# Performance work log

Hardware: AMD Instinct MI355X
Metric: run time of the kernel (lower is better)

## Reference

```python
import jax, jax.numpy as jnp
import numpy as np

N, D, NUM_CLASSES = 8192, 512, 100

def _col_normalize(z):
    # torch.std default is unbiased (ddof=1)
    mean = z.mean(axis=0)
    std = z.std(axis=0, ddof=1)
    return (z - mean) / std

def setup_inputs() -> dict:
    key = jax.random.key(0)
    k1, k2, k3 = jax.random.split(key, 3)
    z_a = jax.random.normal(k1, (N, D), dtype=jnp.float32)
    z_b = jax.random.normal(k2, (N, D), dtype=jnp.float32)
    labels = jax.random.randint(k3, (N,), 0, NUM_CLASSES, dtype=jnp.int64)
    return {"z_a": z_a, "z_b": z_b, "labels": labels}

def reference(z_a, z_b, labels):
    d = z_a.shape[1]
    z_a_norm = _col_normalize(z_a)
    z_b_norm = _col_normalize(z_b)
    # c: [N, N] cross-correlation between samples
    c = jnp.matmul(z_a_norm, z_b_norm.T) / d
    # m[i, j] = 1 if labels[i] == labels[j] else 0 (replaces per-row loop)
    m = (labels[:, None] == labels[None, :]).astype(c.dtype)
    loss = jnp.sum((c - m) ** 2)
    return loss
```

## Files before the change

kernel.cpp:

```cpp
#include <hip/hip_runtime.h>
#include <math.h>


#define NN 8192
#define DD 512
#define NC 100
#define SPLITK 16
#define NXT 10
#define NTILE 14

#define CPS_B   0u
#define CPQ_B   524288u
#define MUA_B   1048576u
#define MUB_B   1050624u
#define RSA_B   1052672u
#define RSB_B   1054720u
#define CNT_B   1056768u
#define XTA_B   4194304u
#define XTB_B   12582912u
#define MT_B    20971520u
#define PART_B  23068672u

typedef __attribute__((ext_vector_type(8))) short short8;
typedef __attribute__((ext_vector_type(4))) float f32x4;

__constant__ int c_ti[NTILE] = {0,0,0,0,1,1,1,2,2,3, 0,1,2,3};
__constant__ int c_tj[NTILE] = {0,1,2,3,1,2,3,2,3,3, 4,4,4,4};
__constant__ float c_w[NXT]  = {1.f,2.f,2.f,2.f,1.f,2.f,2.f,1.f,2.f,1.f};

#if defined(__has_builtin)
#if __has_builtin(__builtin_amdgcn_global_load_lds)
#define HAVE_GLL 1
#endif
#endif

#ifdef HAVE_GLL
__device__ __forceinline__ void async16(const void* g, void* l) {
    __builtin_amdgcn_global_load_lds(
        (const __attribute__((address_space(1))) void*)g,
        (__attribute__((address_space(3))) void*)l, 16, 0, 0);
}
#endif

__device__ __forceinline__ short f2bf_rne(float f) {
    unsigned int u = __builtin_bit_cast(unsigned int, f);
    u += 0x7fffu + ((u >> 16) & 1u);
    return (short)(u >> 16);
}

__device__ __forceinline__ float block_reduce_sum_p(float v, float* red) {
    int lane = threadIdx.x & 63;
    int wave = threadIdx.x >> 6;
    #pragma unroll
    for (int off = 32; off > 0; off >>= 1) v += __shfl_down(v, off, 64);
    if (lane == 0) red[wave] = v;
    __syncthreads();
    float s = 0.f;
    if (threadIdx.x == 0) {
        int nw = (blockDim.x + 63) >> 6;
        for (int w = 0; w < nw; w++) s += red[w];
    }
    return s;
}

__global__ __launch_bounds__(256) void k_prep(const float* __restrict__ A,
                                              const float* __restrict__ B,
                                              const int* __restrict__ labels,
                                              short* __restrict__ XTa,
                                              short* __restrict__ XTb,
                                              short* __restrict__ MT,
                                              float* __restrict__ cpsum,
                                              float* __restrict__ cpsq,
                                              int* __restrict__ counts,
                                              float* __restrict__ out) {
    __shared__ short LT[64][72];
    __shared__ float WS[4][16][4];
    __shared__ float WQ[4][16][4];
    __shared__ int hist[NC];
    int bid = blockIdx.x;
    int t = threadIdx.x;

    if (bid >= 2048) {
        if (bid >= 2176) {
            if (t < NC) hist[t] = 0;
            __syncthreads();
            for (int i = t; i < NN; i += 256) atomicAdd(&hist[labels[i]], 1);
            __syncthreads();
            if (t < 128) counts[t] = (t < NC) ? hist[t] : 0;
            if (t == 0) out[0] = 0.f;
            return;
        }
        int c = bid - 2048;
        unsigned short one = 0x3F80;
        ushort4* dst = (ushort4*)(MT + (size_t)c * NN);
        const int4* lb4 = (const int4*)labels;
        #pragma unroll
        for (int j = 0; j < 8; j++) {
            int i4 = j * 256 + t;
            int4 lb = lb4[i4];
            ushort4 v;
            v.x = (lb.x == c) ? one : (unsigned short)0;
            v.y = (lb.y == c) ? one : (unsigned short)0;
            v.z = (lb.z == c) ? one : (unsigned short)0;
            v.w = (lb.w == c) ? one : (unsigned short)0;
            dst[i4] = v;
        }
        return;
    }

    int mat = bid >> 10;
    const float* X = mat ? B : A;
    short* XT = mat ? XTb : XTa;
    int rem = bid & 1023;
    int c0 = (rem >> 7) << 6;
    int kb_blk = rem & 127;
    int k0 = kb_blk << 6;
    int cc = t & 15;
    int kb = t >> 4;

    float4 ps = make_float4(0.f, 0.f, 0.f, 0.f);
    float4 pq = make_float4(0.f, 0.f, 0.f, 0.f);
    #pragma unroll
    for (int s = 0; s < 4; s++) {
        int kr = kb + s * 16;
        float4 v = *(const float4*)&X[(size_t)(k0 + kr) * DD + c0 + cc * 4];
        LT[cc * 4 + 0][kr] = f2bf_rne(v.x);
        LT[cc * 4 + 1][kr] = f2bf_rne(v.y);
        LT[cc * 4 + 2][kr] = f2bf_rne(v.z);
        LT[cc * 4 + 3][kr] = f2bf_rne(v.w);
        ps.x += v.x; ps.y += v.y; ps.z += v.z; ps.w += v.w;
        pq.x += v.x * v.x; pq.y += v.y * v.y;
        pq.z += v.z * v.z; pq.w += v.w * v.w;
    }
    #pragma unroll
    for (int off = 16; off <= 32; off <<= 1) {
        ps.x += __shfl_xor(ps.x, off, 64); pq.x += __shfl_xor(pq.x, off, 64);
        ps.y += __shfl_xor(ps.y, off, 64); pq.y += __shfl_xor(pq.y, off, 64);
        ps.z += __shfl_xor(ps.z, off, 64); pq.z += __shfl_xor(pq.z, off, 64);
        ps.w += __shfl_xor(ps.w, off, 64); pq.w += __shfl_xor(pq.w, off, 64);
    }
    int wv = t >> 6, lane = t & 63;
    if (lane < 16) {
        WS[wv][lane][0] = ps.x; WS[wv][lane][1] = ps.y;
        WS[wv][lane][2] = ps.z; WS[wv][lane][3] = ps.w;
        WQ[wv][lane][0] = pq.x; WQ[wv][lane][1] = pq.y;
        WQ[wv][lane][2] = pq.z; WQ[wv][lane][3] = pq.w;
    }
    __syncthreads();

    #pragma unroll
    for (int s = 0; s < 2; s++) {
        int idx = s * 256 + t;
        int orow = idx >> 3;
        int och = idx & 7;
        *(uint4*)&XT[(size_t)(c0 + orow) * NN + k0 + och * 8] =
            *(const uint4*)&LT[orow][och * 8];
    }
    if (t < 64) {
        int ccf = t >> 2, j = t & 3;
        float s = WS[0][ccf][j] + WS[1][ccf][j] + WS[2][ccf][j] + WS[3][ccf][j];
        float q = WQ[0][ccf][j] + WQ[1][ccf][j] + WQ[2][ccf][j] + WQ[3][ccf][j];
        size_t base = ((size_t)mat * 128 + kb_blk) * 512 + c0 + t;
        cpsum[base] = s;
        cpsq[base] = q;
    }
}

__global__ __launch_bounds__(256, 2) void k_gram(const short* __restrict__ XTa,
                                                 const short* __restrict__ XTb,
                                                 const short* __restrict__ MT,
                                                 float* __restrict__ part,
                                                 const float* __restrict__ cpsum,
                                                 const float* __restrict__ cpsq,
                                                 float* __restrict__ mu_a,
                                                 float* __restrict__ mu_b,
                                                 float* __restrict__ rs_a,
                                                 float* __restrict__ rs_b) {
    __shared__ short LA[2][128 * 64];
    __shared__ short LB[2][128 * 64];

    int b = blockIdx.x;
    int t = threadIdx.x;

    if (b >= 448) {
        int mat = b - 448;
        for (int k = t; k < DD; k += 256) {
            float s = 0.f, q = 0.f;
            for (int kb = 0; kb < 128; kb++) {
                size_t base = ((size_t)mat * 128 + kb) * 512 + k;
                s += cpsum[base];
                q += cpsq[base];
            }
            float mu = s * (1.0f / (float)NN);
            float var = (q - (float)NN * mu * mu) / (float)(NN - 1);
            (mat ? mu_b : mu_a)[k] = mu;
            (mat ? rs_b : rs_a)[k] = rsqrtf(var);
        }
        return;
    }

    int xcd = b & 7;
    int idx = b >> 3;
    int grp = (idx / NTILE) * 8 + xcd;
    int tile = idx % NTILE;
    int mat = grp >> 4;
    int chunk = grp & 15;

    const short* XT = mat ? XTb : XTa;
    int ti = c_ti[tile], tj = c_tj[tile];
    const short* PA = XT + (size_t)ti * 128 * NN;
    const short* PB = (tj < 4) ? (XT + (size_t)tj * 128 * NN) : MT;
    int k0 = chunk * (NN / SPLITK);

    int wave = t >> 6, lane = t & 63;
    int quad = lane >> 4, l16 = lane & 15;
    int x7 = l16 & 7;
    int wrow = (wave >> 1) * 64, wcol = (wave & 1) * 64;

    int srow = lane >> 3;
    int sc = (lane & 7) ^ srow;

    auto stage = [&](int buf, int kk) {
        #pragma unroll
        for (int rr = 0; rr < 4; rr++) {
            int seg = wave * 4 + rr;
            int row = seg * 8 + srow;
            const short* ga = PA + (size_t)row * NN + k0 + kk + sc * 8;
            const short* gb = PB + (size_t)row * NN + k0 + kk + sc * 8;
#ifdef HAVE_GLL
            async16(ga, &LA[buf][seg * 512]);
            async16(gb, &LB[buf][seg * 512]);
#else
            *(uint4*)&LA[buf][seg * 512 + lane * 8] = *(const uint4*)ga;
            *(uint4*)&LB[buf][seg * 512 + lane * 8] = *(const uint4*)gb;
#endif
        }
    };

    f32x4 acc[4][4];
    #pragma unroll
    for (int i = 0; i < 4; i++)
        #pragma unroll
        for (int j = 0; j < 4; j++) acc[i][j] = (f32x4)0.f;

    const int KR = NN / SPLITK;
    int cur = 0;
    stage(0, 0);
    __syncthreads();

    for (int kk = 0; kk < KR; kk += 64) {
        if (kk + 64 < KR) stage(cur ^ 1, kk + 64);
        #pragma unroll
        for (int ks = 0; ks < 2; ks++) {
            short8 a[4], bfr[4];
            #pragma unroll
            for (int mt = 0; mt < 4; mt++)
                a[mt] = *(const short8*)&LA[cur][(wrow + mt * 16 + l16) * 64 +
                                                 (((ks * 4 + quad) ^ x7) << 3)];
            #pragma unroll
            for (int nt = 0; nt < 4; nt++)
                bfr[nt] = *(const short8*)&LB[cur][(wcol + nt * 16 + l16) * 64 +
                                                   (((ks * 4 + quad) ^ x7) << 3)];
            #pragma unroll
            for (int mt = 0; mt < 4; mt++)
                #pragma unroll
                for (int nt = 0; nt < 4; nt++)
                    acc[mt][nt] = __builtin_amdgcn_mfma_f32_16x16x32_bf16(
                        a[mt], bfr[nt], acc[mt][nt], 0, 0, 0);
        }
        __syncthreads();
        cur ^= 1;
    }

    float* pbase = part + ((size_t)(mat * NTILE + tile) * SPLITK + chunk) * 16384;
    #pragma unroll
    for (int mt = 0; mt < 4; mt++)
        #pragma unroll
        for (int nt = 0; nt < 4; nt++)
            #pragma unroll
            for (int rj = 0; rj < 4; rj++) {
                int rr2 = wrow + mt * 16 + quad * 4 + rj;
                int cc2 = wcol + nt * 16 + l16;
                pbase[rr2 * 128 + cc2] = acc[mt][nt][rj];
            }
}

__global__ __launch_bounds__(256) void k_reduce(const float* __restrict__ part,
                                                const float* __restrict__ mu_a,
                                                const float* __restrict__ mu_b,
                                                const float* __restrict__ rs_a,
                                                const float* __restrict__ rs_b,
                                                const int* __restrict__ counts,
                                                float* __restrict__ out) {
    __shared__ float red[8];
    int bid = blockIdx.x;
    int tile = bid >> 5, sub = bid & 31;
    int t = threadIdx.x;
    int e2 = sub * 512 + t * 2;

    const float2* pa = (const float2*)(part +
        ((size_t)tile * SPLITK) * 16384 + e2);
    const float2* pb = (const float2*)(part +
        ((size_t)(NTILE + tile) * SPLITK) * 16384 + e2);
    float2 Sa = make_float2(0.f, 0.f);
    float2 Sb = make_float2(0.f, 0.f);
    #pragma unroll
    for (int c = 0; c < SPLITK; c++) {
        float2 va = pa[(size_t)c * 8192];
        float2 vb = pb[(size_t)c * 8192];
        Sa.x += va.x; Sa.y += va.y;
        Sb.x += vb.x; Sb.y += vb.y;
    }

    int rw = e2 >> 7, cl = e2 & 127;
    float local = 0.f;
    float scale;
    if (tile < NXT) {
        int gi = c_ti[tile] * 128 + rw;
        int gj = c_tj[tile] * 128 + cl;
        float mai = mu_a[gi], rai = rs_a[gi];
        float mbi = mu_b[gi], rbi = rs_b[gi];
        float2 maj = *(const float2*)&mu_a[gj];
        float2 raj = *(const float2*)&rs_a[gj];
        float2 mbj = *(const float2*)&mu_b[gj];
        float2 rbj = *(const float2*)&rs_b[gj];
        float ga, gb;
        ga = rai * raj.x * (Sa.x - (float)NN * mai * maj.x);
        gb = rbi * rbj.x * (Sb.x - (float)NN * mbi * mbj.x);
        local += ga * gb;
        ga = rai * raj.y * (Sa.y - (float)NN * mai * maj.y);
        gb = rbi * rbj.y * (Sb.y - (float)NN * mbi * mbj.y);
        local += ga * gb;
        scale = c_w[tile] * (1.0f / ((float)DD * (float)DD));
    } else {
        int k = (tile - NXT) * 128 + rw;
        float mak = mu_a[k], rak = rs_a[k];
        float mbk = mu_b[k], rbk = rs_b[k];
        int2 cn = *(const int2*)&counts[cl];
        float ta, tb;
        ta = rak * (Sa.x - (float)cn.x * mak);
        tb = rbk * (Sb.x - (float)cn.x * mbk);
        local += ta * tb;
        ta = rak * (Sa.y - (float)cn.y * mak);
        tb = rbk * (Sb.y - (float)cn.y * mbk);
        local += ta * tb;
        scale = -2.0f / (float)DD;
    }

    float s = block_reduce_sum_p(local, red);
    if (t == 0) {
        float add = s * scale;
        if (bid == 0) {
            float t3 = 0.f;
            for (int cc2 = 0; cc2 < NC; cc2++) {
                float nc = (float)counts[cc2];
                t3 += nc * nc;
            }
            add += t3;
        }
        atomicAdd(out, add);
    }
}

extern "C" void kernel_launch(void* const* d_in, const int* in_sizes, int n_in,
                              void* d_out, int out_size, void* d_ws, size_t ws_size,
                              hipStream_t stream) {
    const float* z_a = (const float*)d_in[0];
    const float* z_b = (const float*)d_in[1];
    const int* labels = (const int*)d_in[2];
    float* out = (float*)d_out;
    char* wsb = (char*)d_ws;

    float* cpsum = (float*)(wsb + CPS_B);
    float* cpsq = (float*)(wsb + CPQ_B);
    float* mu_a = (float*)(wsb + MUA_B);
    float* mu_b = (float*)(wsb + MUB_B);
    float* rs_a = (float*)(wsb + RSA_B);
    float* rs_b = (float*)(wsb + RSB_B);
    int* counts = (int*)(wsb + CNT_B);
    short* XTa = (short*)(wsb + XTA_B);
    short* XTb = (short*)(wsb + XTB_B);
    short* MT = (short*)(wsb + MT_B);
    float* part = (float*)(wsb + PART_B);

    hipLaunchKernelGGL(k_prep, dim3(2177), dim3(256), 0, stream,
                       z_a, z_b, labels, XTa, XTb, MT, cpsum, cpsq, counts, out);
    hipLaunchKernelGGL(k_gram, dim3(450), dim3(256), 0, stream,
                       XTa, XTb, MT, part, cpsum, cpsq, mu_a, mu_b, rs_a, rs_b);
    hipLaunchKernelGGL(k_reduce, dim3(448), dim3(256), 0, stream,
                       part, mu_a, mu_b, rs_a, rs_b, counts, out);
}
```

Before: 110.3 us.

## Fuse split-K reduction into gram kernel via last-block atomic counters

Removes the separate k_reduce launch. Each gram block increments a per-tile atomic counter, and the last-arriving block for a tile waits on a flag set by the stats blocks before reducing all split-K partials for that tile. This saves one kernel launch and its tail. The cost is that only 14 blocks do the whole reduction, each looping over 32 sub-chunks serially, and stats readiness is handled by spin-waiting.

```diff
diff --git a/kernel.cpp b/kernel.cpp
--- a/kernel.cpp
+++ b/kernel.cpp
@@ -16,6 +16,7 @@
 #define RSA_B   1052672u
 #define RSB_B   1054720u
 #define CNT_B   1056768u
+#define FLG_B   1057280u
 #define XTA_B   4194304u
 #define XTB_B   12582912u
 #define MT_B    20971520u
@@ -72,6 +73,7 @@
                                               float* __restrict__ cpsum,
                                               float* __restrict__ cpsq,
                                               int* __restrict__ counts,
+                                              int* __restrict__ flg,
                                               float* __restrict__ out) {
     __shared__ short LT[64][72];
     __shared__ float WS[4][16][4];
@@ -87,6 +89,7 @@
             for (int i = t; i < NN; i += 256) atomicAdd(&hist[labels[i]], 1);
             __syncthreads();
             if (t < 128) counts[t] = (t < NC) ? hist[t] : 0;
+            if (t < 16) flg[t] = 0;
             if (t == 0) out[0] = 0.f;
             return;
         }
@@ -175,9 +178,14 @@
                                                  float* __restrict__ mu_a,
                                                  float* __restrict__ mu_b,
                                                  float* __restrict__ rs_a,
-                                                 float* __restrict__ rs_b) {
+                                                 float* __restrict__ rs_b,
+                                                 const int* __restrict__ counts,
+                                                 int* __restrict__ flg,
+                                                 float* __restrict__ out) {
     __shared__ short LA[2][128 * 64];
     __shared__ short LB[2][128 * 64];
+    __shared__ float red[8];
+    __shared__ int lastflag;
 
     int b = blockIdx.x;
     int t = threadIdx.x;
@@ -195,6 +203,11 @@
             float var = (q - (float)NN * mu * mu) / (float)(NN - 1);
             (mat ? mu_b : mu_a)[k] = mu;
             (mat ? rs_b : rs_a)[k] = rsqrtf(var);
+        }
+        __syncthreads();
+        if (t == 0) {
+            __threadfence();
+            atomicAdd(&flg[14], 1);
         }
         return;
     }
@@ -283,74 +296,79 @@
                 int cc2 = wcol + nt * 16 + l16;
                 pbase[rr2 * 128 + cc2] = acc[mt][nt][rj];
             }
-}
-
-__global__ __launch_bounds__(256) void k_reduce(const float* __restrict__ part,
-                                                const float* __restrict__ mu_a,
-                                                const float* __restrict__ mu_b,
-                                                const float* __restrict__ rs_a,
-                                                const float* __restrict__ rs_b,
-                                                const int* __restrict__ counts,
-                                                float* __restrict__ out) {
-    __shared__ float red[8];
-    int bid = blockIdx.x;
-    int tile = bid >> 5, sub = bid & 31;
-    int t = threadIdx.x;
-    int e2 = sub * 512 + t * 2;
-
-    const float2* pa = (const float2*)(part +
-        ((size_t)tile * SPLITK) * 16384 + e2);
-    const float2* pb = (const float2*)(part +
-        ((size_t)(NTILE + tile) * SPLITK) * 16384 + e2);
-    float2 Sa = make_float2(0.f, 0.f);
-    float2 Sb = make_float2(0.f, 0.f);
-    #pragma unroll
-    for (int c = 0; c < SPLITK; c++) {
-        float2 va = pa[(size_t)c * 8192];
-        float2 vb = pb[(size_t)c * 8192];
-        Sa.x += va.x; Sa.y += va.y;
-        Sb.x += vb.x; Sb.y += vb.y;
-    }
-
-    int rw = e2 >> 7, cl = e2 & 127;
+
+    __syncthreads();
+    if (t == 0) {
+        __threadfence();
+        int old = atomicAdd(&flg[tile], 1);
+        lastflag = (old == 2 * SPLITK - 1);
+    }
+    __syncthreads();
+    if (!lastflag) return;
+
+    if (t == 0) {
+        while (__hip_atomic_load(&flg[14], __ATOMIC_ACQUIRE,
+                                 __HIP_MEMORY_SCOPE_AGENT) < 2)
+            __builtin_amdgcn_s_sleep(8);
+    }
+    __syncthreads();
+    __threadfence();
+
+    const float* pA = part + ((size_t)(0 * NTILE + tile) * SPLITK) * 16384;
+    const float* pB = part + ((size_t)(1 * NTILE + tile) * SPLITK) * 16384;
     float local = 0.f;
     float scale;
-    if (tile < NXT) {
-        int gi = c_ti[tile] * 128 + rw;
-        int gj = c_tj[tile] * 128 + cl;
-        float mai = mu_a[gi], rai = rs_a[gi];
-        float mbi = mu_b[gi], rbi = rs_b[gi];
-        float2 maj = *(const float2*)&mu_a[gj];
-        float2 raj = *(const float2*)&rs_a[gj];
-        float2 mbj = *(const float2*)&mu_b[gj];
-        float2 rbj = *(const float2*)&rs_b[gj];
-        float ga, gb;
-        ga = rai * raj.x * (Sa.x - (float)NN * mai * maj.x);
-        gb = rbi * rbj.x * (Sb.x - (float)NN * mbi * mbj.x);
-        local += ga * gb;
-        ga = rai * raj.y * (Sa.y - (float)NN * mai * maj.y);
-        gb = rbi * rbj.y * (Sb.y - (float)NN * mbi * mbj.y);
-        local += ga * gb;
-        scale = c_w[tile] * (1.0f / ((float)DD * (float)DD));
-    } else {
-        int k = (tile - NXT) * 128 + rw;
-        float mak = mu_a[k], rak = rs_a[k];
-        float mbk = mu_b[k], rbk = rs_b[k];
-        int2 cn = *(const int2*)&counts[cl];
-        float ta, tb;
-        ta = rak * (Sa.x - (float)cn.x * mak);
-        tb = rbk * (Sb.x - (float)cn.x * mbk);
-        local += ta * tb;
-        ta = rak * (Sa.y - (float)cn.y * mak);
-        tb = rbk * (Sb.y - (float)cn.y * mbk);
-        local += ta * tb;
-        scale = -2.0f / (float)DD;
+    if (tile < NXT) scale = c_w[tile] * (1.0f / ((float)DD * (float)DD));
+    else            scale = -2.0f / (float)DD;
+
+    #pragma unroll 1
+    for (int sub = 0; sub < 32; sub++) {
+        int e2 = sub * 512 + t * 2;
+        float2 Sa = make_float2(0.f, 0.f);
+        float2 Sb = make_float2(0.f, 0.f);
+        #pragma unroll
+        for (int c = 0; c < SPLITK; c++) {
+            float2 va = *(const float2*)&pA[(size_t)c * 16384 + e2];
+            float2 vb = *(const float2*)&pB[(size_t)c * 16384 + e2];
+            Sa.x += va.x; Sa.y += va.y;
+            Sb.x += vb.x; Sb.y += vb.y;
+        }
+        int rw = e2 >> 7, cl = e2 & 127;
+        if (tile < NXT) {
+            int gi = c_ti[tile] * 128 + rw;
+            int gj = c_tj[tile] * 128 + cl;
+            float mai = mu_a[gi], rai = rs_a[gi];
+            float mbi = mu_b[gi], rbi = rs_b[gi];
+            float2 maj = *(const float2*)&mu_a[gj];
+            float2 raj = *(const float2*)&rs_a[gj];
+            float2 mbj = *(const float2*)&mu_b[gj];
+            float2 rbj = *(const float2*)&rs_b[gj];
+            float ga, gb;
+            ga = rai * raj.x * (Sa.x - (float)NN * mai * maj.x);
+            gb = rbi * rbj.x * (Sb.x - (float)NN * mbi * mbj.x);
+            local += ga * gb;
+            ga = rai * raj.y * (Sa.y - (float)NN * mai * maj.y);
+            gb = rbi * rbj.y * (Sb.y - (float)NN * mbi * mbj.y);
+            local += ga * gb;
+        } else {
+            int k = (tile - NXT) * 128 + rw;
+            float mak = mu_a[k], rak = rs_a[k];
+            float mbk = mu_b[k], rbk = rs_b[k];
+            int2 cn = *(const int2*)&counts[cl];
+            float ta, tb;
+            ta = rak * (Sa.x - (float)cn.x * mak);
+            tb = rbk * (Sb.x - (float)cn.x * mbk);
+            local += ta * tb;
+            ta = rak * (Sa.y - (float)cn.y * mak);
+            tb = rbk * (Sb.y - (float)cn.y * mbk);
+            local += ta * tb;
+        }
     }
 
     float s = block_reduce_sum_p(local, red);
     if (t == 0) {
         float add = s * scale;
-        if (bid == 0) {
+        if (tile == 0) {
             float t3 = 0.f;
             for (int cc2 = 0; cc2 < NC; cc2++) {
                 float nc = (float)counts[cc2];
@@ -378,15 +396,16 @@
     float* rs_a = (float*)(wsb + RSA_B);
     float* rs_b = (float*)(wsb + RSB_B);
     int* counts = (int*)(wsb + CNT_B);
+    int* flg = (int*)(wsb + FLG_B);
     short* XTa = (short*)(wsb + XTA_B);
     short* XTb = (short*)(wsb + XTB_B);
     short* MT = (short*)(wsb + MT_B);
     float* part = (float*)(wsb + PART_B);
 
     hipLaunchKernelGGL(k_prep, dim3(2177), dim3(256), 0, stream,
-                       z_a, z_b, labels, XTa, XTb, MT, cpsum, cpsq, counts, out);
+                       z_a, z_b, labels, XTa, XTb, MT, cpsum, cpsq,
+                       counts, flg, out);
     hipLaunchKernelGGL(k_gram, dim3(450), dim3(256), 0, stream,
-                       XTa, XTb, MT, part, cpsum, cpsq, mu_a, mu_b, rs_a, rs_b);
-    hipLaunchKernelGGL(k_reduce, dim3(448), dim3(256), 0, stream,
-                       part, mu_a, mu_b, rs_a, rs_b, counts, out);
-}
+                       XTa, XTb, MT, part, cpsum, cpsq,
+                       mu_a, mu_b, rs_a, rs_b, counts, flg, out);
+}
```

Result: slower. 160.6 us (+45.6%).
